# Kernel optimization log

Hardware: AMD Instinct MI355X
Metric: run time of the kernel (lower is better)

## Reference

```python
import jax, jax.numpy as jnp
import numpy as np

D_MODEL, N_LEVELS, N_HEADS, N_POINTS = 256, 4, 8, 4
HEAD_DIM = D_MODEL // N_HEADS
SPATIAL = np.array([[128, 128], [64, 64], [32, 32], [16, 16]], dtype=np.int64)
STARTS = np.concatenate([[0], np.cumsum(SPATIAL[:, 0] * SPATIAL[:, 1])[:-1]]).astype(np.int64)
N_TOK = int((SPATIAL[:, 0] * SPATIAL[:, 1]).sum())  # 21760
B, NQ = 2, 8192


def setup_inputs() -> dict:
    key = jax.random.key(0)
    ks = jax.random.split(key, 12)
    s = 1.0 / np.sqrt(D_MODEL)
    return {
        "query": jax.random.normal(ks[0], (B, NQ, D_MODEL), jnp.float32),
        "reference_points": jax.random.uniform(ks[1], (B, NQ, N_LEVELS, 2), jnp.float32),
        "input_flatten": jax.random.normal(ks[2], (B, N_TOK, D_MODEL), jnp.float32),
        "input_spatial_shapes": jnp.asarray(SPATIAL),
        "input_level_start_index": jnp.asarray(STARTS),
        "Wq": jax.random.normal(ks[3], (D_MODEL, D_MODEL), jnp.float32) * s,
        "bq": jnp.zeros((D_MODEL,), jnp.float32),
        "Wv": jax.random.normal(ks[4], (D_MODEL, D_MODEL), jnp.float32) * s,
        "bv": jnp.zeros((D_MODEL,), jnp.float32),
        "Wa": jax.random.normal(ks[5], (D_MODEL, N_HEADS * N_LEVELS * N_POINTS), jnp.float32) * s,
        "ba": jnp.zeros((N_HEADS * N_LEVELS * N_POINTS,), jnp.float32),
        "sampling_loc": jax.random.uniform(ks[6], (N_HEADS, N_LEVELS, N_POINTS, 2), jnp.float32, -0.1, 0.1),
        "Wo": jax.random.normal(ks[7], (D_MODEL, D_MODEL), jnp.float32) * s,
        "bo": jnp.zeros((D_MODEL,), jnp.float32),
    }


def _bilinear_sample(v_flat, grid, Hl, Wl):
    # v_flat: [B, H, Hl*Wl, Dh]; grid: [B, Nq, H, P, 2] in [-1, 1]
    b, nq, h, p, _ = grid.shape
    gx, gy = grid[..., 0], grid[..., 1]
    # align_corners=False pixel coordinates
    ix = ((gx + 1.0) * Wl - 1.0) * 0.5
    iy = ((gy + 1.0) * Hl - 1.0) * 0.5
    x0f, y0f = jnp.floor(ix), jnp.floor(iy)
    x0, y0 = x0f.astype(jnp.int32), y0f.astype(jnp.int32)
    x1, y1 = x0 + 1, y0 + 1
    wx1, wy1 = ix - x0f, iy - y0f
    wx0, wy0 = 1.0 - wx1, 1.0 - wy1

    def t(a):  # [B,Nq,H,P] -> [B,H,Nq*P]
        return a.transpose(0, 2, 1, 3).reshape(b, h, nq * p)

    def corner(yi, xi, w):
        valid = (xi >= 0) & (xi < Wl) & (yi >= 0) & (yi < Hl)
        idx = jnp.clip(yi, 0, Hl - 1) * Wl + jnp.clip(xi, 0, Wl - 1)
        g = jnp.take_along_axis(v_flat, t(idx)[..., None], axis=2)  # [B,H,Nq*P,Dh]
        return g * t(w * valid.astype(w.dtype))[..., None]

    out = (corner(y0, x0, wy0 * wx0) + corner(y0, x1, wy0 * wx1)
           + corner(y1, x0, wy1 * wx0) + corner(y1, x1, wy1 * wx1))
    return out.reshape(b, h, nq, p, -1)  # [B,H,Nq,P,Dh]


def reference(query, reference_points, input_flatten, input_spatial_shapes,
              input_level_start_index, Wq, bq, Wv, bv, Wa, ba, sampling_loc, Wo, bo):
    b, nq, c = query.shape
    h, L, p, _ = sampling_loc.shape
    dh = c // h
    q = query @ Wq + bq                                   # [B,Nq,C]
    attn = (q @ Wa + ba).reshape(b, nq, h, L, p)
    attn = jax.nn.softmax(attn, axis=-1)                  # softmax over points per level
    v = (input_flatten @ Wv + bv).reshape(b, -1, h, dh)   # [B,N,H,Dh]
    loc = reference_points[:, :, None, :, None, :] + sampling_loc[None, None]  # [B,Nq,H,L,P,2]
    grid = 2.0 * loc - 1.0
    shapes = np.asarray(input_spatial_shapes)
    starts = np.asarray(input_level_start_index)
    samples = []
    for lvl in range(L):
        Hl, Wl = int(shapes[lvl, 0]), int(shapes[lvl, 1])
        s0 = int(starts[lvl])
        vl = v[:, s0:s0 + Hl * Wl].transpose(0, 2, 1, 3)  # [B,H,Hl*Wl,Dh]
        samples.append(_bilinear_sample(vl, grid[:, :, :, lvl], Hl, Wl))
    samples = jnp.stack(samples, axis=3)                  # [B,H,Nq,L,P,Dh]
    out = jnp.einsum('bhnlpd,bnhlp->bnhd', samples, attn).reshape(b, nq, c)
    return out @ Wo + bo
```

## Files before the change

### kernel.cpp

```cpp
#include <hip/hip_runtime.h>
#include <hip/hip_bf16.h>

#define BATCH 2
#define NQ 8192
#define NTOK 21760

typedef __attribute__((ext_vector_type(4))) float f32x4;
typedef __attribute__((ext_vector_type(8))) short s16x8;

static __device__ __forceinline__ unsigned short f2bu(float x) {
    __hip_bfloat16 h = __float2bfloat16(x);
    return __builtin_bit_cast(unsigned short, h);
}

__global__ __launch_bounds__(256) void prep_kernel(
    const float* __restrict__ Wq, const float* __restrict__ Wa,
    const float* __restrict__ bq, const float* __restrict__ ba,
    const float* __restrict__ Wv, const float* __restrict__ Wo,
    unsigned short* __restrict__ WqaT, float* __restrict__ bqa,
    unsigned short* __restrict__ WvT, unsigned short* __restrict__ WoT) {
    const int bid = blockIdx.x;
    const int tid = threadIdx.x;
    if (bid < 128) {
        __shared__ float t[32][33];
        const int mat = bid >> 6;
        const int tile = bid & 63;
        const int i0 = (tile >> 3) * 32, j0 = (tile & 7) * 32;
        const float* src = mat ? Wo : Wv;
        unsigned short* dst = mat ? WoT : WvT;
        const int tx = tid & 31, ty = tid >> 5;
#pragma unroll
        for (int r = 0; r < 4; ++r)
            t[ty + 8 * r][tx] = src[(i0 + ty + 8 * r) * 256 + j0 + tx];
        __syncthreads();
#pragma unroll
        for (int r = 0; r < 4; ++r)
            dst[(j0 + ty + 8 * r) * 256 + i0 + tx] = f2bu(t[tx][ty + 8 * r]);
    } else {
        __shared__ float red[256];
        const int i = bid - 128;
        const int j = tid & 127, kh = tid >> 7;
        float acc = 0.f;
#pragma unroll 8
        for (int k = kh * 128; k < kh * 128 + 128; ++k)
            acc += Wq[i * 256 + k] * Wa[k * 128 + j];
        red[tid] = acc;
        __syncthreads();
        if (kh == 0) {
            WqaT[j * 256 + i] = f2bu(red[j] + red[j + 128]);
            if (i == 0) {
                float b = ba[j];
#pragma unroll 8
                for (int k = 0; k < 256; ++k) b += bq[k] * Wa[k * 128 + j];
                bqa[j] = b;
            }
        }
    }
}

__global__ __launch_bounds__(256) void gemm_vlog(
    const float* __restrict__ inflat, const unsigned short* __restrict__ WvT,
    const float* __restrict__ bv, unsigned short* __restrict__ vbuf,
    const float* __restrict__ query, const unsigned short* __restrict__ WqaT,
    const float* __restrict__ bqa, float* __restrict__ logits) {
    constexpr int K = 256, NT = 4, RA = 4, RB = 4, IM = 4, JN = 4;
    __shared__ __align__(16) char As[128 * 128];
    __shared__ __align__(16) char Bs[128 * 128];
    const int bid = blockIdx.x;
    const float* A;
    const unsigned short* Bt;
    const float* bias;
    int bm, bn, N;
    bool b16;
    if (bid < 680) {
        A = inflat; Bt = WvT; bias = bv;
        bm = (bid >> 1) * 128; bn = (bid & 1) * 128; N = 256; b16 = true;
    } else {
        A = query; Bt = WqaT; bias = bqa;
        bm = (bid - 680) * 128; bn = 0; N = 128; b16 = false;
    }
    const int tid = threadIdx.x;
    const int lane = tid & 63;
    const int wave = tid >> 6;
    const int wr = wave >> 1, wc = wave & 1;
    const int srow = tid >> 3;
    const int skc = (tid & 7) * 8;

    f32x4 acc[IM][JN] = {};
    float4 af0[2][RA], af1[2][RA];
    s16x8 bb[2][RB];

    auto loadT = [&](int t, int buf) {
        const int k0 = t * 64;
#pragma unroll
        for (int r = 0; r < RA; ++r) {
            const float* Af = A + (size_t)(bm + srow + r * 32) * K + k0 + skc;
            af0[buf][r] = *(const float4*)Af;
            af1[buf][r] = *(const float4*)(Af + 4);
        }
#pragma unroll
        for (int r = 0; r < RB; ++r)
            bb[buf][r] = *(const s16x8*)(Bt + (size_t)(bn + srow + r * 32) * K + k0 + skc);
    };
    auto writeT = [&](int buf) {
#pragma unroll
        for (int r = 0; r < RA; ++r) {
            const int row = srow + r * 32;
            const int byte = (row * 128 + skc * 2) ^ ((row & 7) << 4);
            const float4 f0 = af0[buf][r], f1 = af1[buf][r];
            s16x8 av;
            av[0] = (short)f2bu(f0.x); av[1] = (short)f2bu(f0.y);
            av[2] = (short)f2bu(f0.z); av[3] = (short)f2bu(f0.w);
            av[4] = (short)f2bu(f1.x); av[5] = (short)f2bu(f1.y);
            av[6] = (short)f2bu(f1.z); av[7] = (short)f2bu(f1.w);
            *(s16x8*)(As + byte) = av;
        }
#pragma unroll
        for (int r = 0; r < RB; ++r) {
            const int row = srow + r * 32;
            const int byte = (row * 128 + skc * 2) ^ ((row & 7) << 4);
            *(s16x8*)(Bs + byte) = bb[buf][r];
        }
    };

    loadT(0, 0);
#pragma unroll
    for (int t = 0; t < NT; ++t) {
        if (t) __syncthreads();
        if (t + 1 < NT) loadT(t + 1, (t + 1) & 1);
        writeT(t & 1);
        __syncthreads();
#pragma unroll
        for (int f = 0; f < 2; ++f) {
            s16x8 a[IM], b[JN];
#pragma unroll
            for (int i = 0; i < IM; ++i) {
                const int arow = wr * 64 + i * 16 + (lane & 15);
                const int abyte = (arow * 128 + f * 64 + (lane >> 4) * 16) ^ ((arow & 7) << 4);
                a[i] = *(const s16x8*)(As + abyte);
            }
#pragma unroll
            for (int j = 0; j < JN; ++j) {
                const int brow = wc * 64 + j * 16 + (lane & 15);
                const int bbyte = (brow * 128 + f * 64 + (lane >> 4) * 16) ^ ((brow & 7) << 4);
                b[j] = *(const s16x8*)(Bs + bbyte);
            }
#pragma unroll
            for (int i = 0; i < IM; ++i)
#pragma unroll
                for (int j = 0; j < JN; ++j)
                    acc[i][j] = __builtin_amdgcn_mfma_f32_16x16x32_bf16(a[i], b[j], acc[i][j], 0, 0, 0);
        }
    }

#pragma unroll
    for (int i = 0; i < IM; ++i) {
        const int row0 = bm + wr * 64 + i * 16 + (lane >> 4) * 4;
#pragma unroll
        for (int j = 0; j < JN; ++j) {
            const int col = bn + wc * 64 + j * 16 + (lane & 15);
            const float bsv = bias[col];
#pragma unroll
            for (int q = 0; q < 4; ++q) {
                const float val = acc[i][j][q] + bsv;
                if (b16) vbuf[(size_t)(row0 + q) * N + col] = f2bu(val);
                else logits[(size_t)(row0 + q) * N + col] = val;
            }
        }
    }
}

template <int BM, int BN, int WRN, int WCN>
__global__ __launch_bounds__(256) void gemm_out(
    const unsigned short* __restrict__ Av, const unsigned short* __restrict__ Bt,
    const float* __restrict__ bias, float* __restrict__ Cv, int N) {
    constexpr int K = 256, NT = 4;
    constexpr int IM = BM / (WRN * 16);
    constexpr int JN = BN / (WCN * 16);
    constexpr int RA = BM / 32;
    constexpr int RB = BN / 32;
    __shared__ __align__(16) char As[BM * 128];
    __shared__ __align__(16) char Bs[BN * 128];
    const int tid = threadIdx.x;
    const int lane = tid & 63;
    const int wave = tid >> 6;
    const int wr = wave / WCN, wc = wave % WCN;
    const int bm = blockIdx.y * BM, bn = blockIdx.x * BN;
    const int srow = tid >> 3;
    const int skc = (tid & 7) * 8;

    f32x4 acc[IM][JN] = {};
    s16x8 ab[2][RA], bb[2][RB];

    auto loadT = [&](int t, int buf) {
        const int k0 = t * 64;
#pragma unroll
        for (int r = 0; r < RA; ++r)
            ab[buf][r] = *(const s16x8*)(Av + (size_t)(bm + srow + r * 32) * K + k0 + skc);
#pragma unroll
        for (int r = 0; r < RB; ++r)
            bb[buf][r] = *(const s16x8*)(Bt + (size_t)(bn + srow + r * 32) * K + k0 + skc);
    };
    auto writeT = [&](int buf) {
#pragma unroll
        for (int r = 0; r < RA; ++r) {
            const int row = srow + r * 32;
            *(s16x8*)(As + ((row * 128 + skc * 2) ^ ((row & 7) << 4))) = ab[buf][r];
        }
#pragma unroll
        for (int r = 0; r < RB; ++r) {
            const int row = srow + r * 32;
            *(s16x8*)(Bs + ((row * 128 + skc * 2) ^ ((row & 7) << 4))) = bb[buf][r];
        }
    };

    loadT(0, 0);
#pragma unroll
    for (int t = 0; t < NT; ++t) {
        if (t) __syncthreads();
        if (t + 1 < NT) loadT(t + 1, (t + 1) & 1);
        writeT(t & 1);
        __syncthreads();
#pragma unroll
        for (int f = 0; f < 2; ++f) {
            s16x8 a[IM], b[JN];
#pragma unroll
            for (int i = 0; i < IM; ++i) {
                const int arow = wr * (IM * 16) + i * 16 + (lane & 15);
                a[i] = *(const s16x8*)(As + ((arow * 128 + f * 64 + (lane >> 4) * 16) ^ ((arow & 7) << 4)));
            }
#pragma unroll
            for (int j = 0; j < JN; ++j) {
                const int brow = wc * (JN * 16) + j * 16 + (lane & 15);
                b[j] = *(const s16x8*)(Bs + ((brow * 128 + f * 64 + (lane >> 4) * 16) ^ ((brow & 7) << 4)));
            }
#pragma unroll
            for (int i = 0; i < IM; ++i)
#pragma unroll
                for (int j = 0; j < JN; ++j)
                    acc[i][j] = __builtin_amdgcn_mfma_f32_16x16x32_bf16(a[i], b[j], acc[i][j], 0, 0, 0);
        }
    }

#pragma unroll
    for (int i = 0; i < IM; ++i) {
        const int row0 = bm + wr * (IM * 16) + i * 16 + (lane >> 4) * 4;
#pragma unroll
        for (int j = 0; j < JN; ++j) {
            const int col = bn + wc * (JN * 16) + j * 16 + (lane & 15);
            const float bsv = bias[col];
#pragma unroll
            for (int q = 0; q < 4; ++q)
                Cv[(size_t)(row0 + q) * N + col] = acc[i][j][q] + bsv;
        }
    }
}

__global__ __launch_bounds__(256) void sample_kernel(
    const float* __restrict__ refp, const float* __restrict__ sloc,
    const unsigned int* __restrict__ v,
    const float* __restrict__ logits,
    unsigned int* __restrict__ samp) {
    const int tid = threadIdx.x;
    const int q0 = blockIdx.x * 4;
    __shared__ int4 mI[512];
    __shared__ float4 mW[512];
    __shared__ float slc[256];
    __shared__ float lgs[512];
    __shared__ float rps[32];

    {
        const int l = (tid >> 3) & 3;
        slc[tid] = sloc[tid] * (float)(128 >> l) - 0.5f;
    }
    lgs[tid] = logits[(size_t)q0 * 128 + tid];
    lgs[tid + 256] = logits[(size_t)q0 * 128 + tid + 256];
    if (tid < 32) rps[tid] = refp[(size_t)q0 * 8 + tid];
    __syncthreads();

#pragma unroll
    for (int ss = 0; ss < 2; ++ss) {
        const int h = tid & 7;
        const int p = (tid >> 3) & 3;
        const int l = (tid >> 5) & 3;
        const int qi = (tid >> 7) + ss * 2;
        const int lp = l * 4 + p;
        const int b = (q0 + qi) >> 13;
        const int Wl = 128 >> l;
        const float lg = lgs[qi * 128 + h * 16 + lp];
        float m = fmaxf(lg, __shfl_xor(lg, 8));
        m = fmaxf(m, __shfl_xor(m, 16));
        const float e = __expf(lg - m);
        float sum = e + __shfl_xor(e, 8);
        sum += __shfl_xor(sum, 16);
        const float a = e / sum;
        const float fW = (float)Wl;
        const float ix = fmaf(rps[qi * 8 + l * 2 + 0], fW, slc[h * 32 + l * 8 + p * 2 + 0]);
        const float iy = fmaf(rps[qi * 8 + l * 2 + 1], fW, slc[h * 32 + l * 8 + p * 2 + 1]);
        const float xf = floorf(ix), yf = floorf(iy);
        const int x0 = (int)xf, y0 = (int)yf;
        const int x1 = x0 + 1, y1 = y0 + 1;
        float wx1 = ix - xf, wy1 = iy - yf;
        float wx0 = 1.f - wx1, wy0 = 1.f - wy1;
        wx0 = ((unsigned)x0 < (unsigned)Wl) ? wx0 : 0.f;
        wx1 = ((unsigned)x1 < (unsigned)Wl) ? wx1 : 0.f;
        wy0 = ((unsigned)y0 < (unsigned)Wl) ? wy0 * a : 0.f;
        wy1 = ((unsigned)y1 < (unsigned)Wl) ? wy1 * a : 0.f;
        const int x0c = min(max(x0, 0), Wl - 1);
        const int x1c = min(max(x1, 0), Wl - 1);
        const int y0c = min(max(y0, 0), Wl - 1);
        const int y1c = min(max(y1, 0), Wl - 1);
        const int SS = (65536 - (65536 >> (2 * l))) / 3;
        const int base = b * (NTOK * 128) + SS * 128 + h * 16;
        const int r0 = y0c * Wl, r1 = y1c * Wl;
        const int s = lp * 32 + qi * 8 + h;
        mI[s] = make_int4(base + (r0 + x0c) * 128, base + (r0 + x1c) * 128,
                          base + (r1 + x0c) * 128, base + (r1 + x1c) * 128);
        mW[s] = make_float4(wy0 * wx0, wy0 * wx1, wy1 * wx0, wy1 * wx1);
    }
    __syncthreads();

    const int qi = tid >> 6, h = (tid >> 3) & 7, c = tid & 7;
    const int sb = qi * 8 + h;
    const unsigned int* vp = v + c * 2;
    float a0 = 0.f, a1 = 0.f, a2 = 0.f, a3 = 0.f;

    int4 I[2];
    float4 W[2];
    uint2 u[2][4];
    I[0] = mI[sb];
    W[0] = mW[sb];
    u[0][0] = *(const uint2*)(vp + I[0].x);
    u[0][1] = *(const uint2*)(vp + I[0].y);
    u[0][2] = *(const uint2*)(vp + I[0].z);
    u[0][3] = *(const uint2*)(vp + I[0].w);
#pragma unroll
    for (int lp = 0; lp < 16; ++lp) {
        const int cur = lp & 1, nxt = cur ^ 1;
        if (lp < 15) {
            const int s = (lp + 1) * 32 + sb;
            I[nxt] = mI[s];
            W[nxt] = mW[s];
            u[nxt][0] = *(const uint2*)(vp + I[nxt].x);
            u[nxt][1] = *(const uint2*)(vp + I[nxt].y);
            u[nxt][2] = *(const uint2*)(vp + I[nxt].z);
            u[nxt][3] = *(const uint2*)(vp + I[nxt].w);
        }
        const float4 Wc = W[cur];
        a0 = fmaf(__uint_as_float(u[cur][0].x << 16), Wc.x, a0);
        a1 = fmaf(__uint_as_float(u[cur][0].x), Wc.x, a1);
        a2 = fmaf(__uint_as_float(u[cur][0].y << 16), Wc.x, a2);
        a3 = fmaf(__uint_as_float(u[cur][0].y), Wc.x, a3);
        a0 = fmaf(__uint_as_float(u[cur][1].x << 16), Wc.y, a0);
        a1 = fmaf(__uint_as_float(u[cur][1].x), Wc.y, a1);
        a2 = fmaf(__uint_as_float(u[cur][1].y << 16), Wc.y, a2);
        a3 = fmaf(__uint_as_float(u[cur][1].y), Wc.y, a3);
        a0 = fmaf(__uint_as_float(u[cur][2].x << 16), Wc.z, a0);
        a1 = fmaf(__uint_as_float(u[cur][2].x), Wc.z, a1);
        a2 = fmaf(__uint_as_float(u[cur][2].y << 16), Wc.z, a2);
        a3 = fmaf(__uint_as_float(u[cur][2].y), Wc.z, a3);
        a0 = fmaf(__uint_as_float(u[cur][3].x << 16), Wc.w, a0);
        a1 = fmaf(__uint_as_float(u[cur][3].x), Wc.w, a1);
        a2 = fmaf(__uint_as_float(u[cur][3].y << 16), Wc.w, a2);
        a3 = fmaf(__uint_as_float(u[cur][3].y), Wc.w, a3);
    }
    uint2 o;
    o.x = (unsigned)f2bu(a0) | ((unsigned)f2bu(a1) << 16);
    o.y = (unsigned)f2bu(a2) | ((unsigned)f2bu(a3) << 16);
    *(uint2*)(samp + (size_t)(q0 + qi) * 128 + h * 16 + c * 2) = o;
}

extern "C" void kernel_launch(void* const* d_in, const int* in_sizes, int n_in,
                              void* d_out, int out_size, void* d_ws, size_t ws_size,
                              hipStream_t stream) {
    const float* query  = (const float*)d_in[0];
    const float* refp   = (const float*)d_in[1];
    const float* inflat = (const float*)d_in[2];
    const float* Wq = (const float*)d_in[5];
    const float* bq = (const float*)d_in[6];
    const float* Wv = (const float*)d_in[7];
    const float* bv = (const float*)d_in[8];
    const float* Wa = (const float*)d_in[9];
    const float* ba = (const float*)d_in[10];
    const float* sloc = (const float*)d_in[11];
    const float* Wo = (const float*)d_in[12];
    const float* bo = (const float*)d_in[13];
    float* out = (float*)d_out;

    char* ws = (char*)d_ws;
    unsigned short* WqaT = (unsigned short*)(ws + 0);
    float* bqa = (float*)(ws + (64u << 10));
    unsigned short* WvT = (unsigned short*)(ws + (128u << 10));
    unsigned short* WoT = (unsigned short*)(ws + (256u << 10));
    unsigned short* vbuf = (unsigned short*)(ws + (1u << 20));
    float* logits = (float*)(ws + (24u << 20));
    unsigned int* samp = (unsigned int*)(ws + (32u << 20));

    prep_kernel<<<384, 256, 0, stream>>>(Wq, Wa, bq, ba, Wv, Wo, WqaT, bqa, WvT, WoT);
    gemm_vlog<<<808, 256, 0, stream>>>(inflat, WvT, bv, vbuf, query, WqaT, bqa, logits);
    sample_kernel<<<BATCH * NQ / 4, 256, 0, stream>>>(refp, sloc, (const unsigned int*)vbuf, logits, samp);
    gemm_out<64, 128, 1, 4><<<dim3(2, 256), 256, 0, stream>>>((const unsigned short*)samp, WoT, bo, out, 256);
}
```

Before: 204.6 us.

## Sort queries by spatial bucket of reference point before bilinear sampling

Adds a counting sort of queries into 16x16 spatial buckets per batch, keyed on the level-0 reference point. It does this with atomic histogram ranks in the prep kernel, a scan kernel, and a scatter folded into the GEMM launch. The sample kernel then handles queries in permuted order, so neighbouring blocks gather nearby value rows, which should improve L2 and cache locality. The cost is an extra memset and a scan launch, plus indirect loads and stores in the sampler. Reference points are random uniform, so the unsorted order has poor locality.

Measured after the change: 210.8 us. +3.0%, slower.

```diff
diff --git a/kernel.cpp b/kernel.cpp
--- a/kernel.cpp
+++ b/kernel.cpp
@@ -18,7 +18,9 @@
     const float* __restrict__ bq, const float* __restrict__ ba,
     const float* __restrict__ Wv, const float* __restrict__ Wo,
     unsigned short* __restrict__ WqaT, float* __restrict__ bqa,
-    unsigned short* __restrict__ WvT, unsigned short* __restrict__ WoT) {
+    unsigned short* __restrict__ WvT, unsigned short* __restrict__ WoT,
+    const float* __restrict__ refp, int* __restrict__ keys,
+    int* __restrict__ ranks, int* __restrict__ count) {
     const int bid = blockIdx.x;
     const int tid = threadIdx.x;
     if (bid < 128) {
@@ -36,7 +38,7 @@
 #pragma unroll
         for (int r = 0; r < 4; ++r)
             dst[(j0 + ty + 8 * r) * 256 + i0 + tx] = f2bu(t[tx][ty + 8 * r]);
-    } else {
+    } else if (bid < 384) {
         __shared__ float red[256];
         const int i = bid - 128;
         const int j = tid & 127, kh = tid >> 7;
@@ -55,18 +57,50 @@
                 bqa[j] = b;
             }
         }
-    }
+    } else {
+        const int q = (bid - 384) * 256 + tid;
+        const float rx = refp[(size_t)q * 8 + 0];
+        const float ry = refp[(size_t)q * 8 + 1];
+        const int cx = min(15, max(0, (int)(rx * 16.f)));
+        const int cy = min(15, max(0, (int)(ry * 16.f)));
+        const int key = (q >> 13) * 256 + cy * 16 + cx;
+        keys[q] = key;
+        ranks[q] = atomicAdd(&count[key], 1);
+    }
+}
+
+__global__ __launch_bounds__(512) void scan_kernel(const int* __restrict__ count,
+                                                   int* __restrict__ offs) {
+    __shared__ int s[512];
+    const int t = threadIdx.x;
+    const int c = count[t];
+    s[t] = c;
+    __syncthreads();
+    for (int d = 1; d < 512; d <<= 1) {
+        const int v = (t >= d) ? s[t - d] : 0;
+        __syncthreads();
+        s[t] += v;
+        __syncthreads();
+    }
+    offs[t] = s[t] - c;
 }
 
 __global__ __launch_bounds__(256) void gemm_vlog(
     const float* __restrict__ inflat, const unsigned short* __restrict__ WvT,
     const float* __restrict__ bv, unsigned short* __restrict__ vbuf,
     const float* __restrict__ query, const unsigned short* __restrict__ WqaT,
-    const float* __restrict__ bqa, float* __restrict__ logits) {
+    const float* __restrict__ bqa, float* __restrict__ logits,
+    const int* __restrict__ keys, const int* __restrict__ ranks,
+    const int* __restrict__ offs, int* __restrict__ perm) {
     constexpr int K = 256, NT = 4, RA = 4, RB = 4, IM = 4, JN = 4;
     __shared__ __align__(16) char As[128 * 128];
     __shared__ __align__(16) char Bs[128 * 128];
     const int bid = blockIdx.x;
+    if (bid >= 808) {
+        const int q = (bid - 808) * 256 + threadIdx.x;
+        perm[offs[keys[q]] + ranks[q]] = q;
+        return;
+    }
     const float* A;
     const unsigned short* Bt;
     const float* bias;
@@ -260,22 +294,29 @@
     const float* __restrict__ refp, const float* __restrict__ sloc,
     const unsigned int* __restrict__ v,
     const float* __restrict__ logits,
+    const int* __restrict__ perm,
     unsigned int* __restrict__ samp) {
     const int tid = threadIdx.x;
     const int q0 = blockIdx.x * 4;
+    __shared__ int pq[4];
     __shared__ int4 mI[512];
     __shared__ float4 mW[512];
     __shared__ float slc[256];
     __shared__ float lgs[512];
     __shared__ float rps[32];
 
+    if (tid < 4) pq[tid] = perm[q0 + tid];
     {
         const int l = (tid >> 3) & 3;
         slc[tid] = sloc[tid] * (float)(128 >> l) - 0.5f;
     }
-    lgs[tid] = logits[(size_t)q0 * 128 + tid];
-    lgs[tid + 256] = logits[(size_t)q0 * 128 + tid + 256];
-    if (tid < 32) rps[tid] = refp[(size_t)q0 * 8 + tid];
+    __syncthreads();
+#pragma unroll
+    for (int r = 0; r < 2; ++r) {
+        const int qi = (tid >> 7) + 2 * r;
+        lgs[qi * 128 + (tid & 127)] = logits[(size_t)pq[qi] * 128 + (tid & 127)];
+    }
+    if (tid < 32) rps[tid] = refp[(size_t)pq[tid >> 3] * 8 + (tid & 7)];
     __syncthreads();
 
 #pragma unroll
@@ -285,7 +326,7 @@
         const int l = (tid >> 5) & 3;
         const int qi = (tid >> 7) + ss * 2;
         const int lp = l * 4 + p;
-        const int b = (q0 + qi) >> 13;
+        const int b = pq[qi] >> 13;
         const int Wl = 128 >> l;
         const float lg = lgs[qi * 128 + h * 16 + lp];
         float m = fmaxf(lg, __shfl_xor(lg, 8));
@@ -367,7 +408,7 @@
     uint2 o;
     o.x = (unsigned)f2bu(a0) | ((unsigned)f2bu(a1) << 16);
     o.y = (unsigned)f2bu(a2) | ((unsigned)f2bu(a3) << 16);
-    *(uint2*)(samp + (size_t)(q0 + qi) * 128 + h * 16 + c * 2) = o;
+    *(uint2*)(samp + (size_t)pq[qi] * 128 + h * 16 + c * 2) = o;
 }
 
 extern "C" void kernel_launch(void* const* d_in, const int* in_sizes, int n_in,
@@ -395,9 +436,19 @@
     unsigned short* vbuf = (unsigned short*)(ws + (1u << 20));
     float* logits = (float*)(ws + (24u << 20));
     unsigned int* samp = (unsigned int*)(ws + (32u << 20));
-
-    prep_kernel<<<384, 256, 0, stream>>>(Wq, Wa, bq, ba, Wv, Wo, WqaT, bqa, WvT, WoT);
-    gemm_vlog<<<808, 256, 0, stream>>>(inflat, WvT, bv, vbuf, query, WqaT, bqa, logits);
-    sample_kernel<<<BATCH * NQ / 4, 256, 0, stream>>>(refp, sloc, (const unsigned int*)vbuf, logits, samp);
+    int* keys  = (int*)(ws + (40u << 20));
+    int* ranks = (int*)(ws + (40u << 20) + (64u << 10));
+    int* perm  = (int*)(ws + (40u << 20) + (128u << 10));
+    int* count = (int*)(ws + (40u << 20) + (192u << 10));
+    int* offs  = (int*)(ws + (40u << 20) + (194u << 10));
+
+    hipMemsetAsync(count, 0, 512 * sizeof(int), stream);
+    prep_kernel<<<448, 256, 0, stream>>>(Wq, Wa, bq, ba, Wv, Wo, WqaT, bqa, WvT, WoT,
+                                         refp, keys, ranks, count);
+    scan_kernel<<<1, 512, 0, stream>>>(count, offs);
+    gemm_vlog<<<872, 256, 0, stream>>>(inflat, WvT, bv, vbuf, query, WqaT, bqa, logits,
+                                       keys, ranks, offs, perm);
+    sample_kernel<<<BATCH * NQ / 4, 256, 0, stream>>>(refp, sloc, (const unsigned int*)vbuf,
+                                                      logits, perm, samp);
     gemm_out<64, 128, 1, 4><<<dim3(2, 256), 256, 0, stream>>>((const unsigned short*)samp, WoT, bo, out, 256);
 }
```
